# Kernel optimization log

Hardware: AMD Instinct MI355X
Metric: run time of the kernel (lower is better)

The kernel has to match this reference:

```python
import jax, jax.numpy as jnp
import numpy as np

ALPHA = 0.2  # leaky relu negative slope
W_SIZE = 128  # window_size


def setup_inputs() -> dict:
    key = jax.random.key(0)
    ks = jax.random.split(key, 5)
    B, W, K, E = 4, 128, 256, 256  # E = 2*W (gatv2 doubles embed_dim)
    return {
        "x": jax.random.normal(ks[0], (B, W, K), dtype=jnp.float32),
        "lin_w": jax.random.normal(ks[1], (E, 2 * W), dtype=jnp.float32) * (1.0 / np.sqrt(2 * W)),
        "lin_b": jax.random.normal(ks[2], (E,), dtype=jnp.float32) * 0.02,
        "a_vec": jax.random.normal(ks[3], (E,), dtype=jnp.float32) * (1.414 / np.sqrt(E)),
        "bias": jax.random.normal(ks[4], (K, K), dtype=jnp.float32) * 0.02,
    }


def reference(x, lin_w, lin_b, a_vec, bias):
    # x: (B, W, K) -> v: (B, K, W), one W-length vector per node
    v = jnp.transpose(x, (0, 2, 1))
    # GATv2: lin(concat(v_i, v_j)) decomposed: concat @ lin_w.T = v_i @ W1.T + v_j @ W2.T
    W1 = lin_w[:, :W_SIZE]  # (E, W) applied to the repeated (source) block
    W2 = lin_w[:, W_SIZE:]  # (E, W) applied to the alternating (target) block
    u = jnp.einsum("bkw,ew->bke", v, W1)                 # (B, K, E)
    t = jnp.einsum("bkw,ew->bke", v, W2) + lin_b          # (B, K, E)
    pre = u[:, :, None, :] + t[:, None, :, :]             # (B, K, K, E) pairwise
    act = jax.nn.leaky_relu(pre, negative_slope=ALPHA)
    e = jnp.einsum("bije,e->bij", act, a_vec)             # (B, K, K)
    e = e + bias
    attn = jax.nn.softmax(e, axis=-1)
    h = jax.nn.sigmoid(jnp.einsum("bij,bjw->biw", attn, v))  # (B, K, W)
    return jnp.transpose(h, (0, 2, 1))  # (B, W, K)
```

## Files before the change

### kernel.cpp

```cpp
#include <hip/hip_runtime.h>
#include <math.h>

#define NB 4
#define WDIM 128
#define KDIM 256
#define EDIM 256

__global__ __launch_bounds__(256) void k_ut3(const float* __restrict__ x,
                                             const float* __restrict__ lin_w,
                                             const float* __restrict__ lin_b,
                                             float* __restrict__ u_ws,
                                             float* __restrict__ t_ws) {
    __shared__ float vrow[16 * WDIM];
    const int blk = blockIdx.x;
    const int b  = blk >> 6;
    const int kt = (blk >> 2) & 15;
    const int eq = blk & 3;
    const int k0 = kt * 16;
    const int tid = threadIdx.x;
    const int e  = eq * 64 + (tid & 63);
    const int ks = tid >> 6;

    if (tid < WDIM) {
        const float* xp = x + ((size_t)b * WDIM + tid) * KDIM + k0;
#pragma unroll
        for (int q = 0; q < 4; ++q) {
            float4 v = *(const float4*)(xp + q * 4);
            vrow[(q * 4 + 0) * WDIM + tid] = v.x;
            vrow[(q * 4 + 1) * WDIM + tid] = v.y;
            vrow[(q * 4 + 2) * WDIM + tid] = v.z;
            vrow[(q * 4 + 3) * WDIM + tid] = v.w;
        }
    }
    __syncthreads();

    const float4* wr = (const float4*)(lin_w + (size_t)e * 2 * WDIM);
    float uacc[4] = {0.f, 0.f, 0.f, 0.f};
    float tacc[4] = {0.f, 0.f, 0.f, 0.f};
#pragma unroll 8
    for (int q = 0; q < 32; ++q) {
        float4 w1 = wr[q];
        float4 w2 = wr[32 + q];
#pragma unroll
        for (int kk = 0; kk < 4; ++kk) {
            float4 v = *(const float4*)&vrow[(ks * 4 + kk) * WDIM + q * 4];
            uacc[kk] += w1.x * v.x + w1.y * v.y + w1.z * v.z + w1.w * v.w;
            tacc[kk] += w2.x * v.x + w2.y * v.y + w2.z * v.z + w2.w * v.w;
        }
    }
    const float lb = lin_b[e];
#pragma unroll
    for (int kk = 0; kk < 4; ++kk) {
        const int k = k0 + ks * 4 + kk;
        const size_t off = ((size_t)b * KDIM + k) * EDIM + e;
        u_ws[off] = uacc[kk];
        t_ws[off] = tacc[kk] + lb;
    }
}

__global__ __launch_bounds__(256, 1) void k_e3(const float* __restrict__ a_vec,
                                               const float* __restrict__ bias,
                                               const float* __restrict__ u_ws,
                                               const float* __restrict__ t_ws,
                                               float* __restrict__ e_ws) {
    __shared__ float u_lds[8 * 288];
    __shared__ float a_lds[8 * 36];
    const int blk = blockIdx.x;
    const int b     = blk >> 6;
    const int itile = (blk >> 1) & 31;
    const int jh    = blk & 1;
    const int i0 = itile * 8;
    const int tid  = threadIdx.x;
    const int wv   = tid >> 6;
    const int lane = tid & 63;
    const int s  = lane >> 3;
    const int jj = lane & 7;
    const int e_base = s * 32;
    const int j0 = jh * 128 + wv * 32;

    const float* tb = t_ws + (size_t)b * KDIM * EDIM;
    float4 tld[4][8];
#pragma unroll
    for (int jg = 0; jg < 4; ++jg) {
        const float* tr = tb + (size_t)(j0 + jg * 8 + jj) * EDIM + e_base;
#pragma unroll
        for (int q = 0; q < 8; ++q) tld[jg][q] = *(const float4*)(tr + q * 4);
    }

    {
        const int r = tid >> 5;
        const int c = (tid & 31) * 8;
        const int ss = c >> 5, oo = c & 31;
        const float* up = u_ws + ((size_t)b * KDIM + i0 + r) * EDIM + c;
        *(float4*)&u_lds[r * 288 + ss * 36 + oo]     = *(const float4*)up;
        *(float4*)&u_lds[r * 288 + ss * 36 + oo + 4] = *(const float4*)(up + 4);
        if (tid < 64) {
            float4 av = *(const float4*)(a_vec + tid * 4);
            const int s2 = tid >> 3, o2 = (tid & 7) * 4;
            *(float4*)&a_lds[s2 * 36 + o2] =
                make_float4(0.4f * av.x, 0.4f * av.y, 0.4f * av.z, 0.4f * av.w);
        }
    }
    __syncthreads();

    float acc[8][4];
#pragma unroll
    for (int i = 0; i < 8; ++i)
#pragma unroll
        for (int jg = 0; jg < 4; ++jg) acc[i][jg] = 0.f;
    float ru[8] = {0.f,0.f,0.f,0.f,0.f,0.f,0.f,0.f};
    float rt[4] = {0.f,0.f,0.f,0.f};

#pragma unroll
    for (int q = 0; q < 8; ++q) {
        const float4 a2 = *(const float4*)&a_lds[s * 36 + q * 4];
#pragma unroll
        for (int jg = 0; jg < 4; ++jg) {
            const float4 t4 = tld[jg][q];
            rt[jg] += a2.x * t4.x + a2.y * t4.y + a2.z * t4.z + a2.w * t4.w;
        }
#pragma unroll
        for (int i = 0; i < 8; ++i) {
            const float4 u4 = *(const float4*)&u_lds[i * 288 + s * 36 + q * 4];
            ru[i] += a2.x * u4.x + a2.y * u4.y + a2.z * u4.z + a2.w * u4.w;
#pragma unroll
            for (int jg = 0; jg < 4; ++jg) {
                const float4 t4 = tld[jg][q];
                acc[i][jg] += a2.x * fabsf(u4.x + t4.x) + a2.y * fabsf(u4.y + t4.y)
                            + a2.z * fabsf(u4.z + t4.z) + a2.w * fabsf(u4.w + t4.w);
            }
        }
    }

#pragma unroll
    for (int i = 0; i < 8; ++i) {
        ru[i] += __shfl_xor(ru[i], 8, 64);
        ru[i] += __shfl_xor(ru[i], 16, 64);
        ru[i] += __shfl_xor(ru[i], 32, 64);
    }
#pragma unroll
    for (int jg = 0; jg < 4; ++jg) {
        rt[jg] += __shfl_xor(rt[jg], 8, 64);
        rt[jg] += __shfl_xor(rt[jg], 16, 64);
        rt[jg] += __shfl_xor(rt[jg], 32, 64);
    }
#pragma unroll
    for (int i = 0; i < 8; ++i)
#pragma unroll
        for (int jg = 0; jg < 4; ++jg) {
            float v = acc[i][jg];
            v += __shfl_xor(v, 8, 64);
            v += __shfl_xor(v, 16, 64);
            v += __shfl_xor(v, 32, 64);
            acc[i][jg] = v;
        }

    if (s == 0) {
#pragma unroll
        for (int i = 0; i < 8; ++i)
#pragma unroll
            for (int jg = 0; jg < 4; ++jg) {
                const int j = j0 + jg * 8 + jj;
                const float v = acc[i][jg] + 1.5f * (ru[i] + rt[jg])
                              + bias[(size_t)(i0 + i) * KDIM + j];
                e_ws[((size_t)b * KDIM + i0 + i) * KDIM + j] = v;
            }
    }
}

__global__ __launch_bounds__(256) void k_sh3(const float* __restrict__ x,
                                             const float* __restrict__ e_ws,
                                             float* __restrict__ out) {
    __shared__ float attn_lds[4 * 260];
    const int blk = blockIdx.x;
    const int b  = blk >> 6;
    const int i0 = (blk & 63) * 4;
    const int tid  = threadIdx.x;
    const int wv   = tid >> 6;
    const int lane = tid & 63;

    {
        float4 ev = *(const float4*)(e_ws + ((size_t)b * KDIM + i0 + wv) * KDIM + lane * 4);
        float m = fmaxf(fmaxf(ev.x, ev.y), fmaxf(ev.z, ev.w));
#pragma unroll
        for (int o = 1; o < 64; o <<= 1) m = fmaxf(m, __shfl_xor(m, o, 64));
        float4 p;
        p.x = __expf(ev.x - m); p.y = __expf(ev.y - m);
        p.z = __expf(ev.z - m); p.w = __expf(ev.w - m);
        float ssum = p.x + p.y + p.z + p.w;
#pragma unroll
        for (int o = 1; o < 64; o <<= 1) ssum += __shfl_xor(ssum, o, 64);
        const float inv = 1.0f / ssum;
        p.x *= inv; p.y *= inv; p.z *= inv; p.w *= inv;
        *(float4*)&attn_lds[wv * 260 + lane * 4] = p;
    }
    __syncthreads();

    const int js  = lane & 3;
    const int w16 = lane >> 2;
    const float* xb = x + (size_t)b * WDIM * KDIM;
#pragma unroll
    for (int c = 0; c < 2; ++c) {
        const int w = wv * 32 + c * 16 + w16;
        const float* xr = xb + (size_t)w * KDIM;
        float acc[4] = {0.f, 0.f, 0.f, 0.f};
#pragma unroll
        for (int jl = 0; jl < 16; ++jl) {
            const float4 x4 = *(const float4*)(xr + jl * 16 + js * 4);
#pragma unroll
            for (int i = 0; i < 4; ++i) {
                const float4 a4 = *(const float4*)&attn_lds[i * 260 + jl * 16 + js * 4];
                acc[i] += a4.x * x4.x + a4.y * x4.y + a4.z * x4.z + a4.w * x4.w;
            }
        }
#pragma unroll
        for (int i = 0; i < 4; ++i) {
            acc[i] += __shfl_xor(acc[i], 1, 64);
            acc[i] += __shfl_xor(acc[i], 2, 64);
        }
        if (js == 0) {
            float4 o;
            o.x = 1.f / (1.f + __expf(-acc[0]));
            o.y = 1.f / (1.f + __expf(-acc[1]));
            o.z = 1.f / (1.f + __expf(-acc[2]));
            o.w = 1.f / (1.f + __expf(-acc[3]));
            *(float4*)(out + ((size_t)b * WDIM + w) * KDIM + i0) = o;
        }
    }
}

extern "C" void kernel_launch(void* const* d_in, const int* in_sizes, int n_in,
                              void* d_out, int out_size, void* d_ws, size_t ws_size,
                              hipStream_t stream) {
    (void)in_sizes; (void)n_in; (void)out_size; (void)ws_size;
    const float* x     = (const float*)d_in[0];
    const float* lin_w = (const float*)d_in[1];
    const float* lin_b = (const float*)d_in[2];
    const float* a_vec = (const float*)d_in[3];
    const float* bias  = (const float*)d_in[4];
    float* out = (float*)d_out;

    float* u_ws = (float*)d_ws;
    float* t_ws = u_ws + (size_t)NB * KDIM * EDIM;
    float* e_ws = t_ws + (size_t)NB * KDIM * EDIM;

    k_ut3<<<256, 256, 0, stream>>>(x, lin_w, lin_b, u_ws, t_ws);
    k_e3<<<256, 256, 0, stream>>>(a_vec, bias, u_ws, t_ws, e_ws);
    k_sh3<<<256, 256, 0, stream>>>(x, e_ws, out);
}
```

Baseline: 35.43 us.

## Split all three kernels into smaller tiles to launch more blocks

```diff
diff --git a/kernel.cpp b/kernel.cpp
--- a/kernel.cpp
+++ b/kernel.cpp
@@ -6,175 +6,138 @@
 #define KDIM 256
 #define EDIM 256
 
-__global__ __launch_bounds__(256) void k_ut3(const float* __restrict__ x,
+__device__ __forceinline__ float dot4(float4 a, float4 b) {
+    return a.x * b.x + a.y * b.y + a.z * b.z + a.w * b.w;
+}
+
+__global__ __launch_bounds__(256) void k_ut5(const float* __restrict__ x,
                                              const float* __restrict__ lin_w,
                                              const float* __restrict__ lin_b,
                                              float* __restrict__ u_ws,
                                              float* __restrict__ t_ws) {
-    __shared__ float vrow[16 * WDIM];
+    __shared__ float vrow[8 * WDIM];
     const int blk = blockIdx.x;
-    const int b  = blk >> 6;
-    const int kt = (blk >> 2) & 15;
+    const int b  = blk >> 7;
+    const int kt = (blk >> 2) & 31;
     const int eq = blk & 3;
-    const int k0 = kt * 16;
+    const int k0 = kt * 8;
     const int tid = threadIdx.x;
     const int e  = eq * 64 + (tid & 63);
     const int ks = tid >> 6;
 
     if (tid < WDIM) {
         const float* xp = x + ((size_t)b * WDIM + tid) * KDIM + k0;
-#pragma unroll
-        for (int q = 0; q < 4; ++q) {
-            float4 v = *(const float4*)(xp + q * 4);
-            vrow[(q * 4 + 0) * WDIM + tid] = v.x;
-            vrow[(q * 4 + 1) * WDIM + tid] = v.y;
-            vrow[(q * 4 + 2) * WDIM + tid] = v.z;
-            vrow[(q * 4 + 3) * WDIM + tid] = v.w;
-        }
+        float4 v0 = *(const float4*)xp;
+        float4 v1 = *(const float4*)(xp + 4);
+        vrow[0 * WDIM + tid] = v0.x; vrow[1 * WDIM + tid] = v0.y;
+        vrow[2 * WDIM + tid] = v0.z; vrow[3 * WDIM + tid] = v0.w;
+        vrow[4 * WDIM + tid] = v1.x; vrow[5 * WDIM + tid] = v1.y;
+        vrow[6 * WDIM + tid] = v1.z; vrow[7 * WDIM + tid] = v1.w;
     }
     __syncthreads();
 
     const float4* wr = (const float4*)(lin_w + (size_t)e * 2 * WDIM);
-    float uacc[4] = {0.f, 0.f, 0.f, 0.f};
-    float tacc[4] = {0.f, 0.f, 0.f, 0.f};
+    float u0 = 0.f, u1 = 0.f, t0 = 0.f, t1 = 0.f;
 #pragma unroll 8
     for (int q = 0; q < 32; ++q) {
         float4 w1 = wr[q];
         float4 w2 = wr[32 + q];
-#pragma unroll
-        for (int kk = 0; kk < 4; ++kk) {
-            float4 v = *(const float4*)&vrow[(ks * 4 + kk) * WDIM + q * 4];
-            uacc[kk] += w1.x * v.x + w1.y * v.y + w1.z * v.z + w1.w * v.w;
-            tacc[kk] += w2.x * v.x + w2.y * v.y + w2.z * v.z + w2.w * v.w;
-        }
+        float4 va = *(const float4*)&vrow[(ks * 2 + 0) * WDIM + q * 4];
+        float4 vb = *(const float4*)&vrow[(ks * 2 + 1) * WDIM + q * 4];
+        u0 += dot4(w1, va); u1 += dot4(w1, vb);
+        t0 += dot4(w2, va); t1 += dot4(w2, vb);
     }
     const float lb = lin_b[e];
-#pragma unroll
-    for (int kk = 0; kk < 4; ++kk) {
-        const int k = k0 + ks * 4 + kk;
-        const size_t off = ((size_t)b * KDIM + k) * EDIM + e;
-        u_ws[off] = uacc[kk];
-        t_ws[off] = tacc[kk] + lb;
-    }
-}
-
-__global__ __launch_bounds__(256, 1) void k_e3(const float* __restrict__ a_vec,
+    const int k = k0 + ks * 2;
+    const size_t o0 = ((size_t)b * KDIM + k) * EDIM + e;
+    u_ws[o0] = u0;         u_ws[o0 + EDIM] = u1;
+    t_ws[o0] = t0 + lb;    t_ws[o0 + EDIM] = t1 + lb;
+}
+
+__global__ __launch_bounds__(256, 4) void k_e5(const float* __restrict__ a_vec,
                                                const float* __restrict__ bias,
                                                const float* __restrict__ u_ws,
                                                const float* __restrict__ t_ws,
                                                float* __restrict__ e_ws) {
-    __shared__ float u_lds[8 * 288];
-    __shared__ float a_lds[8 * 36];
+    __shared__ float a2_lds[EDIM];
     const int blk = blockIdx.x;
-    const int b     = blk >> 6;
-    const int itile = (blk >> 1) & 31;
-    const int jh    = blk & 1;
-    const int i0 = itile * 8;
+    const int b  = blk >> 8;
+    const int it = (blk >> 3) & 31;
+    const int jt = blk & 7;
+    const int i0 = it * 8;
+    const int j0 = jt * 32;
     const int tid  = threadIdx.x;
     const int wv   = tid >> 6;
     const int lane = tid & 63;
-    const int s  = lane >> 3;
-    const int jj = lane & 7;
-    const int e_base = s * 32;
-    const int j0 = jh * 128 + wv * 32;
+    const int s  = lane & 7;
+    const int jj = lane >> 3;
+    const int iA = i0 + wv * 2;
+
+    if (tid < 64) {
+        float4 av = *(const float4*)(a_vec + tid * 4);
+        *(float4*)&a2_lds[tid * 4] =
+            make_float4(0.4f * av.x, 0.4f * av.y, 0.4f * av.z, 0.4f * av.w);
+    }
+
+    const float* uAp = u_ws + ((size_t)b * KDIM + iA) * EDIM;
+    float4 uA[8], uB[8];
+#pragma unroll
+    for (int q = 0; q < 8; ++q) {
+        uA[q] = *(const float4*)(uAp + q * 32 + s * 4);
+        uB[q] = *(const float4*)(uAp + EDIM + q * 32 + s * 4);
+    }
+    __syncthreads();
+
+    float ruA = 0.f, ruB = 0.f;
+#pragma unroll
+    for (int q = 0; q < 8; ++q) {
+        float4 a2 = *(const float4*)&a2_lds[q * 32 + s * 4];
+        ruA += dot4(a2, uA[q]);
+        ruB += dot4(a2, uB[q]);
+    }
 
     const float* tb = t_ws + (size_t)b * KDIM * EDIM;
-    float4 tld[4][8];
 #pragma unroll
     for (int jg = 0; jg < 4; ++jg) {
-        const float* tr = tb + (size_t)(j0 + jg * 8 + jj) * EDIM + e_base;
-#pragma unroll
-        for (int q = 0; q < 8; ++q) tld[jg][q] = *(const float4*)(tr + q * 4);
-    }
-
-    {
-        const int r = tid >> 5;
-        const int c = (tid & 31) * 8;
-        const int ss = c >> 5, oo = c & 31;
-        const float* up = u_ws + ((size_t)b * KDIM + i0 + r) * EDIM + c;
-        *(float4*)&u_lds[r * 288 + ss * 36 + oo]     = *(const float4*)up;
-        *(float4*)&u_lds[r * 288 + ss * 36 + oo + 4] = *(const float4*)(up + 4);
-        if (tid < 64) {
-            float4 av = *(const float4*)(a_vec + tid * 4);
-            const int s2 = tid >> 3, o2 = (tid & 7) * 4;
-            *(float4*)&a_lds[s2 * 36 + o2] =
-                make_float4(0.4f * av.x, 0.4f * av.y, 0.4f * av.z, 0.4f * av.w);
+        const int j = j0 + jg * 8 + jj;
+        const float* tr = tb + (size_t)j * EDIM;
+        float4 tld[8];
+#pragma unroll
+        for (int q = 0; q < 8; ++q) tld[q] = *(const float4*)(tr + q * 32 + s * 4);
+
+        float accA = 0.f, accB = 0.f, rt = 0.f;
+#pragma unroll
+        for (int q = 0; q < 8; ++q) {
+            float4 a2 = *(const float4*)&a2_lds[q * 32 + s * 4];
+            float4 t4 = tld[q];
+            rt += dot4(a2, t4);
+            accA += a2.x * fabsf(uA[q].x + t4.x) + a2.y * fabsf(uA[q].y + t4.y)
+                  + a2.z * fabsf(uA[q].z + t4.z) + a2.w * fabsf(uA[q].w + t4.w);
+            accB += a2.x * fabsf(uB[q].x + t4.x) + a2.y * fabsf(uB[q].y + t4.y)
+                  + a2.z * fabsf(uB[q].z + t4.z) + a2.w * fabsf(uB[q].w + t4.w);
         }
-    }
-    __syncthreads();
-
-    float acc[8][4];
-#pragma unroll
-    for (int i = 0; i < 8; ++i)
-#pragma unroll
-        for (int jg = 0; jg < 4; ++jg) acc[i][jg] = 0.f;
-    float ru[8] = {0.f,0.f,0.f,0.f,0.f,0.f,0.f,0.f};
-    float rt[4] = {0.f,0.f,0.f,0.f};
-
-#pragma unroll
-    for (int q = 0; q < 8; ++q) {
-        const float4 a2 = *(const float4*)&a_lds[s * 36 + q * 4];
-#pragma unroll
-        for (int jg = 0; jg < 4; ++jg) {
-            const float4 t4 = tld[jg][q];
-            rt[jg] += a2.x * t4.x + a2.y * t4.y + a2.z * t4.z + a2.w * t4.w;
+        float zA = accA + 1.5f * (ruA + rt);
+        float zB = accB + 1.5f * (ruB + rt);
+        zA += __shfl_xor(zA, 1, 64); zB += __shfl_xor(zB, 1, 64);
+        zA += __shfl_xor(zA, 2, 64); zB += __shfl_xor(zB, 2, 64);
+        zA += __shfl_xor(zA, 4, 64); zB += __shfl_xor(zB, 4, 64);
+        if (s == 0) {
+            e_ws[((size_t)b * KDIM + iA) * KDIM + j]     = zA + bias[(size_t)iA * KDIM + j];
+            e_ws[((size_t)b * KDIM + iA + 1) * KDIM + j] = zB + bias[(size_t)(iA + 1) * KDIM + j];
         }
-#pragma unroll
-        for (int i = 0; i < 8; ++i) {
-            const float4 u4 = *(const float4*)&u_lds[i * 288 + s * 36 + q * 4];
-            ru[i] += a2.x * u4.x + a2.y * u4.y + a2.z * u4.z + a2.w * u4.w;
-#pragma unroll
-            for (int jg = 0; jg < 4; ++jg) {
-                const float4 t4 = tld[jg][q];
-                acc[i][jg] += a2.x * fabsf(u4.x + t4.x) + a2.y * fabsf(u4.y + t4.y)
-                            + a2.z * fabsf(u4.z + t4.z) + a2.w * fabsf(u4.w + t4.w);
-            }
-        }
-    }
-
-#pragma unroll
-    for (int i = 0; i < 8; ++i) {
-        ru[i] += __shfl_xor(ru[i], 8, 64);
-        ru[i] += __shfl_xor(ru[i], 16, 64);
-        ru[i] += __shfl_xor(ru[i], 32, 64);
-    }
-#pragma unroll
-    for (int jg = 0; jg < 4; ++jg) {
-        rt[jg] += __shfl_xor(rt[jg], 8, 64);
-        rt[jg] += __shfl_xor(rt[jg], 16, 64);
-        rt[jg] += __shfl_xor(rt[jg], 32, 64);
-    }
-#pragma unroll
-    for (int i = 0; i < 8; ++i)
-#pragma unroll
-        for (int jg = 0; jg < 4; ++jg) {
-            float v = acc[i][jg];
-            v += __shfl_xor(v, 8, 64);
-            v += __shfl_xor(v, 16, 64);
-            v += __shfl_xor(v, 32, 64);
-            acc[i][jg] = v;
-        }
-
-    if (s == 0) {
-#pragma unroll
-        for (int i = 0; i < 8; ++i)
-#pragma unroll
-            for (int jg = 0; jg < 4; ++jg) {
-                const int j = j0 + jg * 8 + jj;
-                const float v = acc[i][jg] + 1.5f * (ru[i] + rt[jg])
-                              + bias[(size_t)(i0 + i) * KDIM + j];
-                e_ws[((size_t)b * KDIM + i0 + i) * KDIM + j] = v;
-            }
-    }
-}
-
-__global__ __launch_bounds__(256) void k_sh3(const float* __restrict__ x,
+    }
+}
+
+__global__ __launch_bounds__(256) void k_sh5(const float* __restrict__ x,
                                              const float* __restrict__ e_ws,
                                              float* __restrict__ out) {
-    __shared__ float attn_lds[4 * 260];
+    __shared__ float attn_lds[4][260];
     const int blk = blockIdx.x;
-    const int b  = blk >> 6;
-    const int i0 = (blk & 63) * 4;
+    const int b  = blk >> 8;
+    const int it = (blk >> 2) & 63;
+    const int wq = blk & 3;
+    const int i0 = it * 4;
+    const int w0 = wq * 32;
     const int tid  = threadIdx.x;
     const int wv   = tid >> 6;
     const int lane = tid & 63;
@@ -192,40 +155,37 @@
         for (int o = 1; o < 64; o <<= 1) ssum += __shfl_xor(ssum, o, 64);
         const float inv = 1.0f / ssum;
         p.x *= inv; p.y *= inv; p.z *= inv; p.w *= inv;
-        *(float4*)&attn_lds[wv * 260 + lane * 4] = p;
+        *(float4*)&attn_lds[wv][lane * 4] = p;
     }
     __syncthreads();
 
-    const int js  = lane & 3;
-    const int w16 = lane >> 2;
-    const float* xb = x + (size_t)b * WDIM * KDIM;
-#pragma unroll
-    for (int c = 0; c < 2; ++c) {
-        const int w = wv * 32 + c * 16 + w16;
-        const float* xr = xb + (size_t)w * KDIM;
-        float acc[4] = {0.f, 0.f, 0.f, 0.f};
-#pragma unroll
-        for (int jl = 0; jl < 16; ++jl) {
-            const float4 x4 = *(const float4*)(xr + jl * 16 + js * 4);
-#pragma unroll
-            for (int i = 0; i < 4; ++i) {
-                const float4 a4 = *(const float4*)&attn_lds[i * 260 + jl * 16 + js * 4];
-                acc[i] += a4.x * x4.x + a4.y * x4.y + a4.z * x4.z + a4.w * x4.w;
-            }
+    const int s  = lane & 7;
+    const int ww = lane >> 3;
+    const int w  = w0 + wv * 8 + ww;
+    const float* xr = x + ((size_t)b * WDIM + w) * KDIM;
+    float acc[4] = {0.f, 0.f, 0.f, 0.f};
+#pragma unroll
+    for (int q = 0; q < 8; ++q) {
+        float4 x4 = *(const float4*)(xr + q * 32 + s * 4);
+#pragma unroll
+        for (int i = 0; i < 4; ++i) {
+            float4 at = *(const float4*)&attn_lds[i][q * 32 + s * 4];
+            acc[i] += dot4(at, x4);
         }
-#pragma unroll
-        for (int i = 0; i < 4; ++i) {
-            acc[i] += __shfl_xor(acc[i], 1, 64);
-            acc[i] += __shfl_xor(acc[i], 2, 64);
-        }
-        if (js == 0) {
-            float4 o;
-            o.x = 1.f / (1.f + __expf(-acc[0]));
-            o.y = 1.f / (1.f + __expf(-acc[1]));
-            o.z = 1.f / (1.f + __expf(-acc[2]));
-            o.w = 1.f / (1.f + __expf(-acc[3]));
-            *(float4*)(out + ((size_t)b * WDIM + w) * KDIM + i0) = o;
-        }
+    }
+#pragma unroll
+    for (int i = 0; i < 4; ++i) {
+        acc[i] += __shfl_xor(acc[i], 1, 64);
+        acc[i] += __shfl_xor(acc[i], 2, 64);
+        acc[i] += __shfl_xor(acc[i], 4, 64);
+    }
+    if (s == 0) {
+        float4 o;
+        o.x = 1.f / (1.f + __expf(-acc[0]));
+        o.y = 1.f / (1.f + __expf(-acc[1]));
+        o.z = 1.f / (1.f + __expf(-acc[2]));
+        o.w = 1.f / (1.f + __expf(-acc[3]));
+        *(float4*)(out + ((size_t)b * WDIM + w) * KDIM + i0) = o;
     }
 }
 
@@ -244,7 +204,7 @@
     float* t_ws = u_ws + (size_t)NB * KDIM * EDIM;
     float* e_ws = t_ws + (size_t)NB * KDIM * EDIM;
 
-    k_ut3<<<256, 256, 0, stream>>>(x, lin_w, lin_b, u_ws, t_ws);
-    k_e3<<<256, 256, 0, stream>>>(a_vec, bias, u_ws, t_ws, e_ws);
-    k_sh3<<<256, 256, 0, stream>>>(x, e_ws, out);
-}
+    k_ut5<<<512, 256, 0, stream>>>(x, lin_w, lin_b, u_ws, t_ws);
+    k_e5<<<1024, 256, 0, stream>>>(a_vec, bias, u_ws, t_ws, e_ws);
+    k_sh5<<<1024, 256, 0, stream>>>(x, e_ws, out);
+}
```

Result: slower. 36.88 us (+4.1%).
